# Performance work log

Measured on AMD Instinct MI355X. Metric: run time of the kernel, lower is better.

## Reference

```python
import jax, jax.numpy as jnp
import numpy as np

N, E, B = 50000, 800000, 2000
EMB, FEAT, L, NTASK = 300, 512, 5, 1
EPS = 1e-5


def setup_inputs() -> dict:
    key = jax.random.key(0)
    ks = jax.random.split(key, 40)
    s = 0.05
    d = {
        'x': jax.random.randint(ks[0], (N, 42), 0, 3),
        'edge_index': jax.random.randint(ks[1], (2, E), 0, N),
        'edge_attr': jax.random.randint(ks[2], (E, 10), 0, 3),
        'batch': jnp.sort(jax.random.randint(ks[3], (N,), 0, B)),
        'x_add': jax.random.normal(ks[4], (B, 200), jnp.float32),
        # atom embeddings
        'atom_e1': jax.random.normal(ks[5], (120, EMB), jnp.float32) * s,
        'atom_e2': jax.random.normal(ks[6], (3, EMB), jnp.float32) * s,
        'atom_w3': jax.random.normal(ks[7], (40, EMB), jnp.float32) * s,
        'atom_b3': jnp.zeros((EMB,), jnp.float32),
        # per-layer GINEConv params (stacked over L layers)
        'edge_e1': jax.random.normal(ks[8], (L, 6, EMB), jnp.float32) * s,
        'edge_e2': jax.random.normal(ks[9], (L, 4, EMB), jnp.float32) * s,
        'edge_w3': jax.random.normal(ks[10], (L, 8, EMB), jnp.float32) * s,
        'edge_b3': jnp.zeros((L, EMB), jnp.float32),
        'mlp_w1': jax.random.normal(ks[11], (L, EMB, 2 * EMB), jnp.float32) * s,
        'mlp_b1': jnp.zeros((L, 2 * EMB), jnp.float32),
        'mlp_w2': jax.random.normal(ks[12], (L, 2 * EMB, EMB), jnp.float32) * s,
        'mlp_b2': jnp.zeros((L, EMB), jnp.float32),
        'bn_g': jnp.ones((L, EMB), jnp.float32),
        'bn_b': jnp.zeros((L, EMB), jnp.float32),
        # feat_lin: emb_dim + 200 -> feat_dim
        'feat_w': jax.random.normal(ks[13], (EMB + 200, FEAT), jnp.float32) * s,
        'feat_b': jnp.zeros((FEAT,), jnp.float32),
        # pred head: 512->256 softplus, 256->256 softplus, 256->1
        'pw1': jax.random.normal(ks[14], (FEAT, FEAT // 2), jnp.float32) * s,
        'pb1': jnp.zeros((FEAT // 2,), jnp.float32),
        'pw2': jax.random.normal(ks[15], (FEAT // 2, FEAT // 2), jnp.float32) * s,
        'pb2': jnp.zeros((FEAT // 2,), jnp.float32),
        'pw3': jax.random.normal(ks[16], (FEAT // 2, NTASK), jnp.float32) * s,
        'pb3': jnp.zeros((NTASK,), jnp.float32),
    }
    return d


def reference(x, edge_index, edge_attr, batch, x_add,
              atom_e1, atom_e2, atom_w3, atom_b3,
              edge_e1, edge_e2, edge_w3, edge_b3,
              mlp_w1, mlp_b1, mlp_w2, mlp_b2, bn_g, bn_b,
              feat_w, feat_b, pw1, pb1, pw2, pb2, pw3, pb3):
    n = x.shape[0]
    nb = x_add.shape[0]

    # node embedding: emb(atom_type) + emb(chirality) + Linear(40 float feats)
    h = (atom_e1[x[:, 0]] + atom_e2[x[:, 1]]
         + x[:, 2:].astype(jnp.float32) @ atom_w3 + atom_b3)

    # add self loops once (same for every layer); self-loop attr: col0=4, rest 0
    loop = jnp.arange(n, dtype=edge_index.dtype)
    src = jnp.concatenate([edge_index[0], loop])
    dst = jnp.concatenate([edge_index[1], loop])
    ea0 = jnp.concatenate([edge_attr[:, 0], jnp.full((n,), 4, edge_attr.dtype)])
    ea1 = jnp.concatenate([edge_attr[:, 1], jnp.zeros((n,), edge_attr.dtype)])
    eaf = jnp.concatenate([edge_attr[:, 2:].astype(jnp.float32),
                           jnp.zeros((n, 8), jnp.float32)], axis=0)

    for l in range(L):
        e_emb = edge_e1[l][ea0] + edge_e2[l][ea1] + eaf @ edge_w3[l] + edge_b3[l]
        msg = h[src] + e_emb                              # [E+N, EMB] gather
        agg = jax.ops.segment_sum(msg, dst, num_segments=n)  # scatter-add
        h = jnp.maximum(agg @ mlp_w1[l] + mlp_b1[l], 0.0) @ mlp_w2[l] + mlp_b2[l]
        # BatchNorm1d (training-mode batch stats, biased var)
        mu = jnp.mean(h, axis=0)
        var = jnp.mean((h - mu) ** 2, axis=0)
        h = (h - mu) * jax.lax.rsqrt(var + EPS) * bn_g[l] + bn_b[l]
        if l != L - 1:
            h = jnp.maximum(h, 0.0)
    h_node = h

    # global mean pool per graph
    sums = jax.ops.segment_sum(h_node, batch, num_segments=nb)
    cnt = jax.ops.segment_sum(jnp.ones((n, 1), h_node.dtype), batch, num_segments=nb)
    pooled = sums / jnp.maximum(cnt, 1.0)

    g = jnp.concatenate([pooled, x_add], axis=1) @ feat_w + feat_b
    g = jax.nn.softplus(g @ pw1 + pb1)
    g = jax.nn.softplus(g @ pw2 + pb2)
    pred = g @ pw3 + pb3
    return h_node, pred
```

## Files before the change

kernel.cpp:

```cpp
#include <hip/hip_runtime.h>
#include <stdint.h>

#define NN 50000
#define EE 800000
#define BG 2000
#define EMB 300
#define HP 320
#define YP 640
#define MPAD 50048
#define MHEAD 2048
#define NLAYER 5

typedef __attribute__((ext_vector_type(8))) _Float16 f16x8;
typedef __attribute__((ext_vector_type(4))) float f32x4;

__device__ __forceinline__ _Float16 f2h(float f) { return (_Float16)f; }

__global__ void k_tconv_all(const float* __restrict__ mw1, const float* __restrict__ mw2,
        const float* __restrict__ fw, const float* __restrict__ pw1, const float* __restrict__ pw2,
        _Float16* __restrict__ w1t, _Float16* __restrict__ w2t, _Float16* __restrict__ fwt,
        _Float16* __restrict__ p1t, _Float16* __restrict__ p2t) {
    int job = blockIdx.x;
    const float* src; _Float16* dst; int K, Ns, Kp, Np;
    if (job < 5)       { src = mw1 + (size_t)job * EMB * 2 * EMB; dst = w1t + (size_t)job * YP * HP; K = EMB; Ns = 2 * EMB; Kp = HP; Np = YP; }
    else if (job < 10) { int l = job - 5; src = mw2 + (size_t)l * 2 * EMB * EMB; dst = w2t + (size_t)l * HP * YP; K = 2 * EMB; Ns = EMB; Kp = YP; Np = HP; }
    else if (job == 10){ src = fw;  dst = fwt; K = 500; Ns = 512; Kp = 512; Np = 512; }
    else if (job == 11){ src = pw1; dst = p1t; K = 512; Ns = 256; Kp = 512; Np = 256; }
    else               { src = pw2; dst = p2t; K = 256; Ns = 256; Kp = 256; Np = 256; }
    int total = Kp * Np;
    for (int idx = blockIdx.y * 256 + threadIdx.x; idx < total; idx += gridDim.y * 256) {
        int n = idx / Kp, k = idx - n * Kp;
        float v = (n < Ns && k < K) ? src[(size_t)k * Ns + n] : 0.f;
        dst[idx] = f2h(v);
    }
}

__global__ void k_padbias_all(const float* __restrict__ mb1, const float* __restrict__ mb2,
                              float* __restrict__ b1p, float* __restrict__ b2p) {
    int idx = blockIdx.x * 256 + threadIdx.x;
    if (idx < NLAYER * YP) {
        int l = idx / YP, c = idx - l * YP;
        b1p[idx] = (c < 2 * EMB) ? mb1[(size_t)l * 2 * EMB + c] : 0.f;
    } else if (idx < NLAYER * YP + NLAYER * HP) {
        int j = idx - NLAYER * YP; int l = j / HP, c = j - l * HP;
        b2p[j] = (c < EMB) ? mb2[(size_t)l * EMB + c] : 0.f;
    }
}

__global__ void k_prep(int* __restrict__ deg, int* __restrict__ cursor,
                       float* __restrict__ psum, float* __restrict__ psq) {
    int i = blockIdx.x * blockDim.x + threadIdx.x;
    if (i < NN) { deg[i] = 0; cursor[i] = 0; }
    if (i < NLAYER * HP) { psum[i] = 0.f; psq[i] = 0.f; }
}

__global__ __launch_bounds__(256) void k_embed(const int* __restrict__ x,
        const float* __restrict__ ae1, const float* __restrict__ ae2,
        const float* __restrict__ aw3, const float* __restrict__ ab3,
        _Float16* __restrict__ h2) {
    int node = blockIdx.x * 4 + (threadIdx.x >> 6);
    int lane = threadIdx.x & 63;
    if (node >= MPAD) return;
    _Float16* outr = h2 + (size_t)node * HP;
    if (node >= NN) {
        #pragma unroll
        for (int j = 0; j < 5; j++) outr[lane + 64 * j] = (_Float16)0.f;
        return;
    }
    const int* xr = x + (size_t)node * 42;
    int x0 = xr[0], x1 = xr[1];
    float acc[5];
    #pragma unroll
    for (int j = 0; j < 5; j++) {
        int c = lane + 64 * j;
        acc[j] = (j < 4 || c < EMB)
               ? (ab3[c] + ae1[(size_t)x0 * EMB + c] + ae2[(size_t)x1 * EMB + c]) : 0.f;
    }
    for (int k = 0; k < 40; k++) {
        float xv = (float)xr[2 + k];
        #pragma unroll
        for (int j = 0; j < 5; j++) {
            int c = lane + 64 * j;
            if (j < 4 || c < EMB) acc[j] = fmaf(xv, aw3[(size_t)k * EMB + c], acc[j]);
        }
    }
    #pragma unroll
    for (int j = 0; j < 5; j++) {
        int c = lane + 64 * j;
        outr[c] = (j < 4 || c < EMB) ? f2h(acc[j]) : (_Float16)0.f;
    }
}

__global__ void k_deg(const int* __restrict__ ei, int* __restrict__ deg) {
    int e = blockIdx.x * blockDim.x + threadIdx.x;
    if (e < EE) atomicAdd(&deg[ei[EE + e]], 1);
}

__global__ __launch_bounds__(1024) void k_scan(const int* __restrict__ deg,
                                               int* __restrict__ rowptr) {
    __shared__ int part[1024];
    int t = threadIdx.x;
    const int chunk = (NN + 1023) / 1024;
    int i0 = t * chunk;
    int i1 = min(i0 + chunk, NN);
    int s = 0;
    for (int i = i0; i < i1; i++) s += deg[i];
    part[t] = s;
    __syncthreads();
    for (int off = 1; off < 1024; off <<= 1) {
        int v = part[t];
        int u = (t >= off) ? part[t - off] : 0;
        __syncthreads();
        part[t] = v + u;
        __syncthreads();
    }
    int run = (t > 0) ? part[t - 1] : 0;
    for (int i = i0; i < i1; i++) { rowptr[i] = run; run += deg[i]; }
    if (t == 1023) rowptr[NN] = part[1023];
}

__global__ void k_fill(const int* __restrict__ ei, const int* __restrict__ ea,
                       const int* __restrict__ rowptr, int* __restrict__ cursor,
                       int* __restrict__ col, unsigned int* __restrict__ eattr) {
    int e = blockIdx.x * blockDim.x + threadIdx.x;
    if (e < EE) {
        int d = ei[EE + e];
        int pos = rowptr[d] + atomicAdd(&cursor[d], 1);
        col[pos] = ei[e];
        unsigned int p = (unsigned int)ea[e * 10 + 0] | ((unsigned int)ea[e * 10 + 1] << 2);
        #pragma unroll
        for (int j = 0; j < 8; j++) p |= (unsigned int)ea[e * 10 + 2 + j] << (4 + 2 * j);
        eattr[pos] = p;
    }
}

__global__ __launch_bounds__(256) void k_sortrows(const int* __restrict__ rowptr,
                                                  int* __restrict__ col) {
    int node = blockIdx.x * 4 + (threadIdx.x >> 6);
    int lane = threadIdx.x & 63;
    if (node >= NN) return;
    int beg = rowptr[node], end = rowptr[node + 1];
    int deg = end - beg;
    if (deg <= 1 || deg > 64) return;
    int v = (lane < deg) ? col[beg + lane] : 0x7fffffff;
    #pragma unroll
    for (int k = 2; k <= 64; k <<= 1) {
        #pragma unroll
        for (int j = k >> 1; j > 0; j >>= 1) {
            int v2 = __shfl_xor(v, j);
            bool keepMin = (((lane & j) == 0) == ((lane & k) == 0));
            v = keepMin ? min(v, v2) : max(v, v2);
        }
    }
    if (lane < deg) col[beg + lane] = v;
}

__global__ __launch_bounds__(256) void k_stats(const int* __restrict__ rowptr,
        const unsigned int* __restrict__ eattr, int* __restrict__ stat) {
    int node = blockIdx.x * 4 + (threadIdx.x >> 6);
    int lane = threadIdx.x & 63;
    if (node >= NN) return;
    int beg = rowptr[node], end = rowptr[node + 1];
    int c0 = 0, c1 = 0, c2 = 0, d1 = 0, d2 = 0;
    int s[8] = {0, 0, 0, 0, 0, 0, 0, 0};
    for (int e = beg + lane; e < end; e += 64) {
        unsigned int p = eattr[e];
        unsigned int a0 = p & 3u, a1 = (p >> 2) & 3u;
        c0 += (a0 == 0); c1 += (a0 == 1); c2 += (a0 == 2);
        d1 += (a1 == 1); d2 += (a1 == 2);
        #pragma unroll
        for (int j = 0; j < 8; j++) s[j] += (int)((p >> (4 + 2 * j)) & 3u);
    }
    #pragma unroll
    for (int off = 32; off; off >>= 1) {
        c0 += __shfl_down(c0, off); c1 += __shfl_down(c1, off); c2 += __shfl_down(c2, off);
        d1 += __shfl_down(d1, off); d2 += __shfl_down(d2, off);
        #pragma unroll
        for (int j = 0; j < 8; j++) s[j] += __shfl_down(s[j], off);
    }
    if (lane == 0) {
        int dg = end - beg;
        int* st = stat + (size_t)node * 20;
        st[0] = c0; st[1] = c1; st[2] = c2; st[3] = 0; st[4] = 1; st[5] = 0;
        st[6] = dg - d1 - d2 + 1; st[7] = d1; st[8] = d2; st[9] = 0;
        #pragma unroll
        for (int j = 0; j < 8; j++) st[10 + j] = s[j];
        st[18] = dg + 1; st[19] = 0;
    }
}

#define AGG_CHUNK 160
template<int RELU>
__global__ __launch_bounds__(320) void k_agg(const _Float16* __restrict__ h2,
        const float* __restrict__ psum, const float* __restrict__ psq,
        const float* __restrict__ bng, const float* __restrict__ bnb,
        const int* __restrict__ stat, const int* __restrict__ rowptr,
        const int* __restrict__ col,
        const float* __restrict__ ee1, const float* __restrict__ ee2,
        const float* __restrict__ ew3, const float* __restrict__ eb3,
        _Float16* __restrict__ agg, int layer) {
    int i = blockIdx.x;
    int tid = threadIdx.x;
    if (i >= NN) { agg[(size_t)i * HP + tid] = (_Float16)0.f; return; }
    __shared__ int ss[20];
    __shared__ int sc[AGG_CHUNK];
    if (tid < 20) ss[tid] = stat[(size_t)i * 20 + tid];
    int c = tid;
    bool ch = c < EMB;
    float scl = 0.f, sft = 0.f;
    if (ch) {
        if (RELU) {
            float mu = psum[(size_t)(layer - 1) * HP + c] * (1.f / NN);
            float var = psq[(size_t)(layer - 1) * HP + c] * (1.f / NN) - mu * mu;
            float g = bng[(size_t)(layer - 1) * EMB + c] * rsqrtf(var + 1e-5f);
            scl = g; sft = bnb[(size_t)(layer - 1) * EMB + c] - mu * g;
        } else { scl = 1.f; sft = 0.f; }
    }
    __syncthreads();
    float acc = 0.f;
    if (ch) {
        const float* e1 = ee1 + (size_t)layer * 6 * EMB;
        const float* e2 = ee2 + (size_t)layer * 4 * EMB;
        const float* w3 = ew3 + (size_t)layer * 8 * EMB;
        float v = eb3[(size_t)layer * EMB + c] * (float)ss[18] + e1[4 * EMB + c];
        v = fmaf((float)ss[0], e1[c], v);
        v = fmaf((float)ss[1], e1[EMB + c], v);
        v = fmaf((float)ss[2], e1[2 * EMB + c], v);
        v = fmaf((float)ss[6], e2[c], v);
        v = fmaf((float)ss[7], e2[EMB + c], v);
        v = fmaf((float)ss[8], e2[2 * EMB + c], v);
        #pragma unroll
        for (int k = 0; k < 8; k++) v = fmaf((float)ss[10 + k], w3[k * EMB + c], v);
        float t = fmaf((float)h2[(size_t)i * HP + c], scl, sft);
        if (RELU) t = fmaxf(t, 0.f);
        acc = v + t;
    }
    int beg = rowptr[i], end = rowptr[i + 1];
    for (int e0 = beg; e0 < end; e0 += AGG_CHUNK) {
        int m = min(AGG_CHUNK, end - e0);
        __syncthreads();
        if (tid < m) sc[tid] = col[e0 + tid];
        __syncthreads();
        if (ch) {
            #pragma unroll 4
            for (int e = 0; e < m; e++) {
                float t = fmaf((float)h2[(size_t)sc[e] * HP + c], scl, sft);
                if (RELU) t = fmaxf(t, 0.f);
                acc += t;
            }
        }
    }
    agg[(size_t)i * HP + tid] = ch ? f2h(acc) : (_Float16)0.f;
}

__global__ __launch_bounds__(256) void k_gemm(const _Float16* __restrict__ A, int lda,
        const _Float16* __restrict__ Wt, int ldw, const float* __restrict__ bias,
        _Float16* __restrict__ C, int ldc, int K, int act, int gridY,
        float* __restrict__ psum, float* __restrict__ psq) {
    __shared__ _Float16 As[2][128 * 32];
    __shared__ _Float16 Bs[2][64 * 32];
    int nwg = gridDim.x;
    int q = nwg >> 3, r = nwg & 7;
    int xcd = blockIdx.x & 7, idx = blockIdx.x >> 3;
    int wg = ((xcd < r) ? xcd * (q + 1) : r * (q + 1) + (xcd - r) * q) + idx;
    int bx = wg / gridY, by = wg - bx * gridY;
    size_t rowBase = (size_t)bx * 128;
    int colBase = by * 64;

    int tid = threadIdx.x, lane = tid & 63, wid = tid >> 6;
    int wr = wid >> 1, wc = wid & 1;
    int srow = tid >> 2, schunk = tid & 3;
    int gchunk = schunk ^ ((srow >> 1) & 3);
    const _Float16* Ab  = A + (rowBase + srow) * (size_t)lda + (gchunk << 3);
    const _Float16* Ab2 = Ab + (size_t)64 * lda;
    const _Float16* Bb  = Wt + ((size_t)colBase + srow) * ldw + (gchunk << 3);
    int ldsbase = wid << 9;

    int lr = lane & 15, lg = lane >> 4;
    int lswz = (lr >> 1) & 3;
    int aoff[4], boff[2];
    #pragma unroll
    for (int m = 0; m < 4; m++) { int rr = wr * 64 + m * 16 + lr; aoff[m] = rr * 32 + ((lg ^ lswz) << 3); }
    #pragma unroll
    for (int n = 0; n < 2; n++) { int rr = wc * 32 + n * 16 + lr; boff[n] = rr * 32 + ((lg ^ lswz) << 3); }

    f32x4 acc[4][2];
    #pragma unroll
    for (int m = 0; m < 4; m++)
        #pragma unroll
        for (int n = 0; n < 2; n++) acc[m][n] = (f32x4){0.f, 0.f, 0.f, 0.f};

    auto stage = [&](int buf, int kt) {
        int o = kt << 5;
        __builtin_amdgcn_global_load_lds(
            (const __attribute__((address_space(1))) void*)(Ab + o),
            (__attribute__((address_space(3))) void*)&As[buf][ldsbase], 16, 0, 0);
        __builtin_amdgcn_global_load_lds(
            (const __attribute__((address_space(1))) void*)(Ab2 + o),
            (__attribute__((address_space(3))) void*)&As[buf][64 * 32 + ldsbase], 16, 0, 0);
        __builtin_amdgcn_global_load_lds(
            (const __attribute__((address_space(1))) void*)(Bb + o),
            (__attribute__((address_space(3))) void*)&Bs[buf][ldsbase], 16, 0, 0);
    };

    int nk = K >> 5;
    stage(0, 0);
    __syncthreads();
    int cur = 0;
    for (int kt = 0; kt < nk; ++kt) {
        if (kt + 1 < nk) stage(cur ^ 1, kt + 1);
        f16x8 af[4], bfr[2];
        #pragma unroll
        for (int m = 0; m < 4; m++) af[m] = *(const f16x8*)&As[cur][aoff[m]];
        #pragma unroll
        for (int n = 0; n < 2; n++) bfr[n] = *(const f16x8*)&Bs[cur][boff[n]];
        #pragma unroll
        for (int m = 0; m < 4; m++)
            #pragma unroll
            for (int n = 0; n < 2; n++)
                acc[m][n] = __builtin_amdgcn_mfma_f32_16x16x32_f16(af[m], bfr[n], acc[m][n], 0, 0, 0);
        __syncthreads();
        cur ^= 1;
    }

    bool dostats = (psum != nullptr);
    float sstat[2] = {0.f, 0.f}, qstat[2] = {0.f, 0.f};
    #pragma unroll
    for (int m = 0; m < 4; m++) {
        #pragma unroll
        for (int n = 0; n < 2; n++) {
            int colg = colBase + wc * 32 + n * 16 + lr;
            float bv = bias[colg];
            #pragma unroll
            for (int rj = 0; rj < 4; rj++) {
                size_t rowg = rowBase + wr * 64 + m * 16 + lg * 4 + rj;
                float v = acc[m][n][rj] + bv;
                if (act == 1) v = fmaxf(v, 0.f);
                else if (act == 2) v = (v > 0.f) ? v + log1pf(expf(-v)) : log1pf(expf(v));
                C[rowg * ldc + colg] = f2h(v);
                if (dostats && rowg < NN) { sstat[n] += v; qstat[n] += v * v; }
            }
        }
    }
    if (dostats) {
        #pragma unroll
        for (int n = 0; n < 2; n++) {
            float s_ = sstat[n], q_ = qstat[n];
            s_ += __shfl_xor(s_, 16); q_ += __shfl_xor(q_, 16);
            s_ += __shfl_xor(s_, 32); q_ += __shfl_xor(q_, 32);
            if (lane < 16) {
                int colg = colBase + wc * 32 + n * 16 + lr;
                atomicAdd(&psum[colg], s_);
                atomicAdd(&psq[colg], q_);
            }
        }
    }
}

__global__ __launch_bounds__(256) void k_bn_apply(const _Float16* __restrict__ h2,
        const float* __restrict__ psum, const float* __restrict__ psq,
        const float* __restrict__ bng, const float* __restrict__ bnb,
        float* __restrict__ out) {
    int node = blockIdx.x * 4 + (threadIdx.x >> 6);
    int lane = threadIdx.x & 63;
    if (node >= NN) return;
    const float* ps = psum + (size_t)(NLAYER - 1) * HP;
    const float* pq = psq  + (size_t)(NLAYER - 1) * HP;
    const float* g_ = bng + (size_t)(NLAYER - 1) * EMB;
    const float* b_ = bnb + (size_t)(NLAYER - 1) * EMB;
    #pragma unroll
    for (int j = 0; j < 5; j++) {
        int c = lane + 64 * j;
        if (j < 4 || c < EMB) {
            float mu = ps[c] * (1.f / NN);
            float var = pq[c] * (1.f / NN) - mu * mu;
            float g = g_[c] * rsqrtf(var + 1e-5f);
            out[(size_t)node * EMB + c] =
                fmaf((float)h2[(size_t)node * HP + c], g, b_[c] - mu * g);
        }
    }
}

__global__ __launch_bounds__(512) void k_pool(const float* __restrict__ hn,
        const int* __restrict__ batch, const float* __restrict__ x_add,
        _Float16* __restrict__ hin) {
    int b = blockIdx.x, c = threadIdx.x;
    if (b >= BG) { hin[(size_t)b * 512 + c] = (_Float16)0.f; return; }
    __shared__ int sb[2];
    if (c < 2) {
        int target = b + c;
        int lo = 0, hi = NN;
        while (lo < hi) { int mid = (lo + hi) >> 1; if (batch[mid] < target) lo = mid + 1; else hi = mid; }
        sb[c] = lo;
    }
    __syncthreads();
    float v = 0.f;
    if (c < EMB) {
        int s = sb[0], e = sb[1];
        float a = 0.f;
        for (int i = s; i < e; i++) a += hn[(size_t)i * EMB + c];
        v = a / (float)max(e - s, 1);
    } else if (c < EMB + 200) {
        v = x_add[(size_t)b * 200 + (c - EMB)];
    }
    hin[(size_t)b * 512 + c] = f2h(v);
}

__global__ __launch_bounds__(64) void k_pred(const _Float16* __restrict__ g3,
        const float* __restrict__ pw3, const float* __restrict__ pb3, float* __restrict__ out) {
    int row = blockIdx.x;
    int lane = threadIdx.x;
    float s = 0.f;
    #pragma unroll
    for (int t = 0; t < 4; t++) {
        int k = lane * 4 + t;
        s += (float)g3[(size_t)row * 256 + k] * pw3[k];
    }
    #pragma unroll
    for (int off = 32; off; off >>= 1) s += __shfl_down(s, off);
    if (lane == 0) out[row] = s + pb3[0];
}

extern "C" void kernel_launch(void* const* d_in, const int* in_sizes, int n_in,
                              void* d_out, int out_size, void* d_ws, size_t ws_size,
                              hipStream_t stream) {
    const int*   x     = (const int*)d_in[0];
    const int*   ei    = (const int*)d_in[1];
    const int*   ea    = (const int*)d_in[2];
    const int*   batch = (const int*)d_in[3];
    const float* x_add = (const float*)d_in[4];
    const float* ae1   = (const float*)d_in[5];
    const float* ae2   = (const float*)d_in[6];
    const float* aw3   = (const float*)d_in[7];
    const float* ab3   = (const float*)d_in[8];
    const float* ee1   = (const float*)d_in[9];
    const float* ee2   = (const float*)d_in[10];
    const float* ew3   = (const float*)d_in[11];
    const float* eb3   = (const float*)d_in[12];
    const float* mw1   = (const float*)d_in[13];
    const float* mb1   = (const float*)d_in[14];
    const float* mw2   = (const float*)d_in[15];
    const float* mb2   = (const float*)d_in[16];
    const float* bng   = (const float*)d_in[17];
    const float* bnb   = (const float*)d_in[18];
    const float* fw    = (const float*)d_in[19];
    const float* fb    = (const float*)d_in[20];
    const float* pw1   = (const float*)d_in[21];
    const float* pb1   = (const float*)d_in[22];
    const float* pw2   = (const float*)d_in[23];
    const float* pb2   = (const float*)d_in[24];
    const float* pw3   = (const float*)d_in[25];
    const float* pb3   = (const float*)d_in[26];
    (void)in_sizes; (void)n_in; (void)out_size; (void)ws_size;
    float* out = (float*)d_out;

    char* p = (char*)d_ws;
    auto take = [&](size_t bytes) -> char* {
        char* r = p; p += (bytes + 255) & ~(size_t)255; return r;
    };
    _Float16*  h2   = (_Float16*)take((size_t)MPAD * HP * 2);
    _Float16*  agg  = (_Float16*)take((size_t)MPAD * HP * 2);
    _Float16*  y1   = (_Float16*)take((size_t)MPAD * YP * 2);
    _Float16*  w1t  = (_Float16*)take((size_t)NLAYER * YP * HP * 2);
    _Float16*  w2t  = (_Float16*)take((size_t)NLAYER * HP * YP * 2);
    _Float16*  fwt  = (_Float16*)take((size_t)512 * 512 * 2);
    _Float16*  p1t  = (_Float16*)take((size_t)256 * 512 * 2);
    _Float16*  p2t  = (_Float16*)take((size_t)256 * 256 * 2);
    float* b1p    = (float*)take((size_t)NLAYER * YP * 4);
    float* b2p    = (float*)take((size_t)NLAYER * HP * 4);
    int* deg      = (int*)take((size_t)NN * 4);
    int* cursor   = (int*)take((size_t)NN * 4);
    int* rowptr   = (int*)take((size_t)(NN + 1) * 4);
    int* col      = (int*)take((size_t)EE * 4);
    unsigned int* eattr = (unsigned int*)take((size_t)EE * 4);
    int* stat     = (int*)take((size_t)NN * 20 * 4);
    float* psum   = (float*)take((size_t)NLAYER * HP * 4);
    float* psq    = (float*)take((size_t)NLAYER * HP * 4);
    char* hb = (char*)y1;
    _Float16* hin = (_Float16*)hb;  hb += (size_t)MHEAD * 512 * 2;
    _Float16* g1  = (_Float16*)hb;  hb += (size_t)MHEAD * 512 * 2;
    _Float16* g2  = (_Float16*)hb;  hb += (size_t)MHEAD * 256 * 2;
    _Float16* g3  = (_Float16*)hb;

    k_prep<<<(NN + 255) / 256, 256, 0, stream>>>(deg, cursor, psum, psq);
    k_tconv_all<<<dim3(13, 1024), 256, 0, stream>>>(mw1, mw2, fw, pw1, pw2, w1t, w2t, fwt, p1t, p2t);
    k_padbias_all<<<19, 256, 0, stream>>>(mb1, mb2, b1p, b2p);
    k_embed<<<(MPAD + 3) / 4, 256, 0, stream>>>(x, ae1, ae2, aw3, ab3, h2);
    k_deg<<<(EE + 255) / 256, 256, 0, stream>>>(ei, deg);
    k_scan<<<1, 1024, 0, stream>>>(deg, rowptr);
    k_fill<<<(EE + 255) / 256, 256, 0, stream>>>(ei, ea, rowptr, cursor, col, eattr);
    k_sortrows<<<(NN + 3) / 4, 256, 0, stream>>>(rowptr, col);
    k_stats<<<(NN + 3) / 4, 256, 0, stream>>>(rowptr, eattr, stat);

    const int MT = MPAD / 128;
    for (int l = 0; l < NLAYER; l++) {
        if (l == 0)
            k_agg<0><<<MPAD, 320, 0, stream>>>(h2, psum, psq, bng, bnb,
                stat, rowptr, col, ee1, ee2, ew3, eb3, agg, l);
        else
            k_agg<1><<<MPAD, 320, 0, stream>>>(h2, psum, psq, bng, bnb,
                stat, rowptr, col, ee1, ee2, ew3, eb3, agg, l);
        k_gemm<<<MT * (YP / 64), 256, 0, stream>>>(
            agg, HP, w1t + (size_t)l * YP * HP, HP, b1p + (size_t)l * YP,
            y1, YP, HP, 1, YP / 64, nullptr, nullptr);
        k_gemm<<<MT * (HP / 64), 256, 0, stream>>>(
            y1, YP, w2t + (size_t)l * HP * YP, YP, b2p + (size_t)l * HP,
            h2, HP, YP, 0, HP / 64, psum + (size_t)l * HP, psq + (size_t)l * HP);
    }
    k_bn_apply<<<(NN + 3) / 4, 256, 0, stream>>>(h2, psum, psq, bng, bnb, out);

    k_pool<<<MHEAD, 512, 0, stream>>>(out, batch, x_add, hin);
    k_gemm<<<(MHEAD / 128) * (512 / 64), 256, 0, stream>>>(hin, 512, fwt, 512, fb, g1, 512, 512, 0, 512 / 64, nullptr, nullptr);
    k_gemm<<<(MHEAD / 128) * (256 / 64), 256, 0, stream>>>(g1, 512, p1t, 512, pb1, g2, 256, 512, 2, 256 / 64, nullptr, nullptr);
    k_gemm<<<(MHEAD / 128) * (256 / 64), 256, 0, stream>>>(g2, 256, p2t, 256, pb2, g3, 256, 256, 2, 256 / 64, nullptr, nullptr);
    k_pred<<<BG, 64, 0, stream>>>(g3, pw3, pb3, out + (size_t)NN * EMB);
}
```

Before: 1.815 ms.

## Precompute BN+ReLU into separate buffer and batch neighbor gathers in aggregation

Moves the BatchNorm+ReLU normalisation out of the per-edge gather loop into a separate per-node kernel that writes a normalised fp16 copy, so aggregation does plain loads and adds. The aggregation loop drops the shared-memory column staging and its barriers, and instead issues 16 independent neighbour loads per iteration to raise memory-level parallelism. It also removes the per-row column sort, which changes the gather access order and float summation order. In exchange there is an extra full-tensor write and read per layer, plus an extra kernel launch.

```diff
diff --git a/kernel.cpp b/kernel.cpp
--- a/kernel.cpp
+++ b/kernel.cpp
@@ -134,27 +134,6 @@
     }
 }
 
-__global__ __launch_bounds__(256) void k_sortrows(const int* __restrict__ rowptr,
-                                                  int* __restrict__ col) {
-    int node = blockIdx.x * 4 + (threadIdx.x >> 6);
-    int lane = threadIdx.x & 63;
-    if (node >= NN) return;
-    int beg = rowptr[node], end = rowptr[node + 1];
-    int deg = end - beg;
-    if (deg <= 1 || deg > 64) return;
-    int v = (lane < deg) ? col[beg + lane] : 0x7fffffff;
-    #pragma unroll
-    for (int k = 2; k <= 64; k <<= 1) {
-        #pragma unroll
-        for (int j = k >> 1; j > 0; j >>= 1) {
-            int v2 = __shfl_xor(v, j);
-            bool keepMin = (((lane & j) == 0) == ((lane & k) == 0));
-            v = keepMin ? min(v, v2) : max(v, v2);
-        }
-    }
-    if (lane < deg) col[beg + lane] = v;
-}
-
 __global__ __launch_bounds__(256) void k_stats(const int* __restrict__ rowptr,
         const unsigned int* __restrict__ eattr, int* __restrict__ stat) {
     int node = blockIdx.x * 4 + (threadIdx.x >> 6);
@@ -189,11 +168,23 @@
     }
 }
 
-#define AGG_CHUNK 160
-template<int RELU>
-__global__ __launch_bounds__(320) void k_agg(const _Float16* __restrict__ h2,
+__global__ __launch_bounds__(320) void k_bnrelu(const _Float16* __restrict__ h2,
         const float* __restrict__ psum, const float* __restrict__ psq,
         const float* __restrict__ bng, const float* __restrict__ bnb,
+        _Float16* __restrict__ r2, int slot) {
+    int i = blockIdx.x, c = threadIdx.x;
+    float scl = 0.f, sft = 0.f;
+    if (c < EMB) {
+        float mu = psum[(size_t)slot * HP + c] * (1.f / NN);
+        float var = psq[(size_t)slot * HP + c] * (1.f / NN) - mu * mu;
+        float g = bng[(size_t)slot * EMB + c] * rsqrtf(var + 1e-5f);
+        scl = g; sft = bnb[(size_t)slot * EMB + c] - mu * g;
+    }
+    float v = fmaxf(fmaf((float)h2[(size_t)i * HP + c], scl, sft), 0.f);
+    r2[(size_t)i * HP + c] = f2h(v);
+}
+
+__global__ __launch_bounds__(320) void k_agg(const _Float16* __restrict__ src,
         const int* __restrict__ stat, const int* __restrict__ rowptr,
         const int* __restrict__ col,
         const float* __restrict__ ee1, const float* __restrict__ ee2,
@@ -203,19 +194,9 @@
     int tid = threadIdx.x;
     if (i >= NN) { agg[(size_t)i * HP + tid] = (_Float16)0.f; return; }
     __shared__ int ss[20];
-    __shared__ int sc[AGG_CHUNK];
     if (tid < 20) ss[tid] = stat[(size_t)i * 20 + tid];
     int c = tid;
     bool ch = c < EMB;
-    float scl = 0.f, sft = 0.f;
-    if (ch) {
-        if (RELU) {
-            float mu = psum[(size_t)(layer - 1) * HP + c] * (1.f / NN);
-            float var = psq[(size_t)(layer - 1) * HP + c] * (1.f / NN) - mu * mu;
-            float g = bng[(size_t)(layer - 1) * EMB + c] * rsqrtf(var + 1e-5f);
-            scl = g; sft = bnb[(size_t)(layer - 1) * EMB + c] - mu * g;
-        } else { scl = 1.f; sft = 0.f; }
-    }
     __syncthreads();
     float acc = 0.f;
     if (ch) {
@@ -231,26 +212,31 @@
         v = fmaf((float)ss[8], e2[2 * EMB + c], v);
         #pragma unroll
         for (int k = 0; k < 8; k++) v = fmaf((float)ss[10 + k], w3[k * EMB + c], v);
-        float t = fmaf((float)h2[(size_t)i * HP + c], scl, sft);
-        if (RELU) t = fmaxf(t, 0.f);
-        acc = v + t;
-    }
+        acc = v;
+    }
+    acc += (float)src[(size_t)i * HP + c];
     int beg = rowptr[i], end = rowptr[i + 1];
-    for (int e0 = beg; e0 < end; e0 += AGG_CHUNK) {
-        int m = min(AGG_CHUNK, end - e0);
-        __syncthreads();
-        if (tid < m) sc[tid] = col[e0 + tid];
-        __syncthreads();
-        if (ch) {
-            #pragma unroll 4
-            for (int e = 0; e < m; e++) {
-                float t = fmaf((float)h2[(size_t)sc[e] * HP + c], scl, sft);
-                if (RELU) t = fmaxf(t, 0.f);
-                acc += t;
-            }
+    for (int e0 = beg; e0 < end; e0 += 16) {
+        int cb[16];
+        #pragma unroll
+        for (int t = 0; t < 16; t++) {
+            int ee = e0 + t;
+            cb[t] = col[(ee < end) ? ee : beg];
         }
-    }
-    agg[(size_t)i * HP + tid] = ch ? f2h(acc) : (_Float16)0.f;
+        float vb[16];
+        #pragma unroll
+        for (int t = 0; t < 16; t++)
+            vb[t] = (float)src[(size_t)cb[t] * HP + c];
+        #pragma unroll
+        for (int t = 0; t < 16; t++)
+            if (e0 + t >= end) vb[t] = 0.f;
+        float s01 = (vb[0] + vb[1]) + (vb[2] + vb[3]);
+        float s23 = (vb[4] + vb[5]) + (vb[6] + vb[7]);
+        float s45 = (vb[8] + vb[9]) + (vb[10] + vb[11]);
+        float s67 = (vb[12] + vb[13]) + (vb[14] + vb[15]);
+        acc += (s01 + s23) + (s45 + s67);
+    }
+    agg[(size_t)i * HP + tid] = f2h(acc);
 }
 
 __global__ __launch_bounds__(256) void k_gemm(const _Float16* __restrict__ A, int lda,
@@ -459,6 +445,7 @@
         char* r = p; p += (bytes + 255) & ~(size_t)255; return r;
     };
     _Float16*  h2   = (_Float16*)take((size_t)MPAD * HP * 2);
+    _Float16*  r2   = (_Float16*)take((size_t)MPAD * HP * 2);
     _Float16*  agg  = (_Float16*)take((size_t)MPAD * HP * 2);
     _Float16*  y1   = (_Float16*)take((size_t)MPAD * YP * 2);
     _Float16*  w1t  = (_Float16*)take((size_t)NLAYER * YP * HP * 2);
@@ -489,17 +476,17 @@
     k_deg<<<(EE + 255) / 256, 256, 0, stream>>>(ei, deg);
     k_scan<<<1, 1024, 0, stream>>>(deg, rowptr);
     k_fill<<<(EE + 255) / 256, 256, 0, stream>>>(ei, ea, rowptr, cursor, col, eattr);
-    k_sortrows<<<(NN + 3) / 4, 256, 0, stream>>>(rowptr, col);
     k_stats<<<(NN + 3) / 4, 256, 0, stream>>>(rowptr, eattr, stat);
 
     const int MT = MPAD / 128;
     for (int l = 0; l < NLAYER; l++) {
-        if (l == 0)
-            k_agg<0><<<MPAD, 320, 0, stream>>>(h2, psum, psq, bng, bnb,
-                stat, rowptr, col, ee1, ee2, ew3, eb3, agg, l);
-        else
-            k_agg<1><<<MPAD, 320, 0, stream>>>(h2, psum, psq, bng, bnb,
-                stat, rowptr, col, ee1, ee2, ew3, eb3, agg, l);
+        const _Float16* src = h2;
+        if (l > 0) {
+            k_bnrelu<<<NN, 320, 0, stream>>>(h2, psum, psq, bng, bnb, r2, l - 1);
+            src = r2;
+        }
+        k_agg<<<MPAD, 320, 0, stream>>>(src, stat, rowptr, col,
+            ee1, ee2, ew3, eb3, agg, l);
         k_gemm<<<MT * (YP / 64), 256, 0, stream>>>(
             agg, HP, w1t + (size_t)l * YP * HP, HP, b1p + (size_t)l * YP,
             y1, YP, HP, 1, YP / 64, nullptr, nullptr);
```

Measured after the change: 1.931 ms. +6.4%, slower.
